# Performance work log

Measured on AMD Instinct MI355X. Metric: run time of the kernel, lower is better.

Reference implementation:

```python
import jax, jax.numpy as jnp
import numpy as np

NEG_SLOPE = 0.2  # PyG GATConv default leaky_relu slope

def gat_conv(x, src, dst, W, a_src, a_dst, bias, N):
    # Linear transform
    h = x @ W                      # [N, D]
    # Per-node attention logits (heads=1)
    al_src = h @ a_src             # [N]
    al_dst = h @ a_dst             # [N]
    e = jax.nn.leaky_relu(al_src[src] + al_dst[dst], NEG_SLOPE)  # [E]
    # Segment softmax over incoming edges of each destination node
    m = jax.ops.segment_max(e, dst, num_segments=N)
    ex = jnp.exp(e - m[dst])
    denom = jax.ops.segment_sum(ex, dst, num_segments=N)
    alpha = ex / denom[dst]        # [E]
    # Weighted scatter-aggregate of source features
    out = jax.ops.segment_sum(h[src] * alpha[:, None], dst, num_segments=N)
    return out + bias

def setup_inputs() -> dict:
    key = jax.random.key(0)
    ks = jax.random.split(key, 10)
    N, E, F_in, H, O = 50000, 800000, 128, 64, 64
    x = jax.random.normal(ks[0], (N, F_in), dtype=jnp.float32)
    edge_index = jax.random.randint(ks[1], (2, E), 0, N, dtype=jnp.int32)
    s = lambda k, shp, fan: jax.random.normal(k, shp, dtype=jnp.float32) / np.sqrt(fan)
    return {
        'x': x, 'edge_index': edge_index,
        'W1': s(ks[2], (F_in, H), F_in), 'a_src1': s(ks[3], (H,), H), 'a_dst1': s(ks[4], (H,), H), 'b1': jnp.zeros((H,), jnp.float32),
        'W2': s(ks[5], (H, O), H), 'a_src2': s(ks[6], (O,), O), 'a_dst2': s(ks[7], (O,), O), 'b2': jnp.zeros((O,), jnp.float32),
    }

def reference(x, edge_index, W1, a_src1, a_dst1, b1, W2, a_src2, a_dst2, b2):
    N = x.shape[0]
    loops = jnp.arange(N, dtype=edge_index.dtype)  # PyG adds self-loops by default
    src = jnp.concatenate([edge_index[0], loops])
    dst = jnp.concatenate([edge_index[1], loops])
    h = gat_conv(x, src, dst, W1, a_src1, a_dst1, b1, N)
    h = jax.nn.relu(h)
    # dropout(p=0.6) is identity in eval mode
    out = gat_conv(h, src, dst, W2, a_src2, a_dst2, b2, N)
    return out
```

## Files before the change

kernel.cpp:

```cpp
#include <hip/hip_runtime.h>
#include <hip/hip_bf16.h>

#define DEV static __device__ __forceinline__

typedef short bf16x8 __attribute__((ext_vector_type(8)));
typedef float f32x4  __attribute__((ext_vector_type(4)));

union U4 { uint4 u; bf16x8 s; };

DEV float b2f(__hip_bfloat16 v) { return __bfloat162float(v); }
DEV float lrelu(float e) { return e > 0.f ? e : 0.2f * e; }

DEV unsigned short f2bu(float f) {
    __hip_bfloat16 b = __float2bfloat16(f);
    return *reinterpret_cast<unsigned short*>(&b);
}
DEV float bu2f(unsigned short u) { return __uint_as_float((unsigned)u << 16); }

DEV float loadF(const void* p, size_t i, int f32) {
    if (f32) return ((const float*)p)[i];
    return b2f(((const __hip_bfloat16*)p)[i]);
}

DEV uint4 pack8(const unsigned short* t) {
    uint4 v;
    v.x = (unsigned)t[0] | ((unsigned)t[1] << 16);
    v.y = (unsigned)t[2] | ((unsigned)t[3] << 16);
    v.z = (unsigned)t[4] | ((unsigned)t[5] << 16);
    v.w = (unsigned)t[6] | ((unsigned)t[7] << 16);
    return v;
}

__global__ __launch_bounds__(256) void k_detect(
    const void* a0, int n0, const void* a1, int n1, const void* a2, int n2,
    const void* a3, int n3, const void* a4, int n4, const void* a5, int n5,
    const void* a6, int n6, const void* a7, int n7, const void* a8, int n8,
    int* __restrict__ flags)
{
    const void* ps[9] = {a0,a1,a2,a3,a4,a5,a6,a7,a8};
    const int   ns[9] = {n0,n1,n2,n3,n4,n5,n6,n7,n8};
    __shared__ int cnt;
    for (int k = 0; k < 9; ++k) {
        if (threadIdx.x == 0) cnt = 0;
        __syncthreads();
        int samples = ns[k] < 256 ? ns[k] : 256;
        if ((int)threadIdx.x < samples) {
            unsigned short u = ((const unsigned short*)ps[k])[threadIdx.x];
            unsigned e = (u >> 7) & 0xFFu;
            bool insane = (e >= 0xC8u) || (e == 0u && (u & 0x7Fu) != 0u);
            if (insane) atomicAdd(&cnt, 1);
        }
        __syncthreads();
        if (threadIdx.x == 0) flags[k] = (cnt >= 1) ? 1 : 0;
        __syncthreads();
    }
}

DEV void edge_sd(int i, int E, const int* __restrict__ src, const int* __restrict__ dst,
                 int& s, int& d) {
    if (i < E) { s = src[i]; d = dst[i]; }
    else       { s = d = i - E; }
}

#define G_BIN 128

__global__ __launch_bounds__(256) void k_binA(
    const int* __restrict__ src, const int* __restrict__ dst,
    int* __restrict__ hist, int E, int EA, int chunk)
{
    __shared__ int cnt[256];
    const int tid = threadIdx.x;
    cnt[tid] = 0;
    __syncthreads();
    const int lo = blockIdx.x * chunk;
    const int hi = min(lo + chunk, EA);
    for (int i = lo + tid; i < hi; i += 256) {
        int s, d; edge_sd(i, E, src, dst, s, d);
        atomicAdd(&cnt[d >> 8], 1);
    }
    __syncthreads();
    hist[blockIdx.x * 256 + tid] = cnt[tid];
}

__global__ __launch_bounds__(256) void k_binB(
    const int* __restrict__ hist, int* __restrict__ offs,
    int* __restrict__ bstart)
{
    __shared__ int sm[256];
    const int tid = threadIdx.x;
    int total = 0;
    for (int blk = 0; blk < G_BIN; ++blk) total += hist[blk * 256 + tid];
    sm[tid] = total;
    __syncthreads();
#pragma unroll
    for (int off = 1; off < 256; off <<= 1) {
        int t = (tid >= off) ? sm[tid - off] : 0;
        __syncthreads();
        sm[tid] += t;
        __syncthreads();
    }
    int b0 = sm[tid] - total;
    bstart[tid] = b0;
    if (tid == 255) bstart[256] = sm[255];
    int run = b0;
    for (int blk = 0; blk < G_BIN; ++blk) {
        offs[blk * 256 + tid] = run;
        run += hist[blk * 256 + tid];
    }
}

__global__ __launch_bounds__(256) void k_binC(
    const int* __restrict__ src, const int* __restrict__ dst,
    const int* __restrict__ offs, unsigned* __restrict__ ebuf,
    int E, int EA, int chunk)
{
    __shared__ int cur[256];
    const int tid = threadIdx.x;
    cur[tid] = offs[blockIdx.x * 256 + tid];
    __syncthreads();
    const int lo = blockIdx.x * chunk;
    const int hi = min(lo + chunk, EA);
    for (int i = lo + tid; i < hi; i += 256) {
        int s, d; edge_sd(i, E, src, dst, s, d);
        int pos = atomicAdd(&cur[d >> 8], 1);
        ebuf[pos] = ((unsigned)(d & 255) << 17) | (unsigned)s;
    }
}

__global__ __launch_bounds__(256) void k_binD(
    const unsigned* __restrict__ ebuf, const int* __restrict__ bstart,
    int* __restrict__ row_ptr, int* __restrict__ col, int N)
{
    __shared__ int cnt[256];
    __shared__ int pfx[256];
    const int tid = threadIdx.x;
    const int b = blockIdx.x;
    const int lo = bstart[b], hi = bstart[b + 1];
    cnt[tid] = 0;
    __syncthreads();
    for (int i = lo + tid; i < hi; i += 256)
        atomicAdd(&cnt[ebuf[i] >> 17], 1);
    __syncthreads();
    const int c = cnt[tid];
    pfx[tid] = c;
    __syncthreads();
#pragma unroll
    for (int off = 1; off < 256; off <<= 1) {
        int t = (tid >= off) ? pfx[tid - off] : 0;
        __syncthreads();
        pfx[tid] += t;
        __syncthreads();
    }
    const int excl = pfx[tid] - c;
    const int d = b * 256 + tid;
    if (d <= N) row_ptr[d] = lo + excl;
    __syncthreads();
    cnt[tid] = lo + excl;
    __syncthreads();
    for (int i = lo + tid; i < hi; i += 256) {
        unsigned v = ebuf[i];
        int pos = atomicAdd(&cnt[v >> 17], 1);
        col[pos] = (int)(v & 0x1FFFFu);
    }
}

__global__ __launch_bounds__(256) void k_gemm1(
    const void* __restrict__ x, const void* __restrict__ W,
    const void* __restrict__ a_s, const void* __restrict__ a_d,
    const int* __restrict__ flags,
    __hip_bfloat16* __restrict__ h, float* __restrict__ als, float* __restrict__ ald,
    int N)
{
    __shared__ __align__(16) unsigned short sMem[2 * 64 * 136];
    __shared__ float sAs[64], sAd[64];
    unsigned short* sA = sMem;
    unsigned short* sB = sMem + 64 * 136;
    float* sOut = (float*)sMem;

    const int tid = threadIdx.x;
    const int row0 = blockIdx.x * 64;
    const int fx = flags[0], fw = flags[1];

    if (tid < 64) sAs[tid] = loadF(a_s, tid, flags[2]);
    else if (tid < 128) sAd[tid - 64] = loadF(a_d, tid - 64, flags[3]);

    if (!fx) {
        const uint4* xg = (const uint4*)x;
#pragma unroll
        for (int it = 0; it < 2; ++it) {
            int g = tid + it * 256;
            int r = g >> 4, c16 = g & 15;
            uint4 v = (row0 + r < N) ? xg[(size_t)(row0 + r) * 16 + c16]
                                     : make_uint4(0, 0, 0, 0);
            *(uint4*)(sA + r * 136 + c16 * 8) = v;
        }
    } else {
        for (int i = tid; i < 64 * 128; i += 256) {
            int r = i >> 7, k = i & 127;
            float v = (row0 + r < N) ? ((const float*)x)[(size_t)(row0 + r) * 128 + k] : 0.f;
            sA[r * 136 + k] = f2bu(v);
        }
    }
    if (!fw) {
        const unsigned short* Wg = (const unsigned short*)W;
        const int n = tid & 63;
        int k0 = (tid >> 6) * 8;
#pragma unroll
        for (int rep = 0; rep < 4; ++rep, k0 += 32) {
            unsigned short t[8];
#pragma unroll
            for (int j = 0; j < 8; ++j) t[j] = Wg[(size_t)(k0 + j) * 64 + n];
            *(uint4*)(sB + n * 136 + k0) = pack8(t);
        }
    } else {
        const float* Wg = (const float*)W;
        for (int i = tid; i < 128 * 64; i += 256) {
            int k = i >> 6, n = i & 63;
            sB[n * 136 + k] = f2bu(Wg[i]);
        }
    }
    __syncthreads();

    const int w = tid >> 6, lane = tid & 63;
    const int m0 = w * 16;
    const int qr = lane >> 4;
    const int lc = lane & 15;

    bf16x8 afrag[4];
#pragma unroll
    for (int c = 0; c < 4; ++c) {
        U4 u; u.u = *(const uint4*)(sA + (m0 + lc) * 136 + c * 32 + qr * 8);
        afrag[c] = u.s;
    }
    f32x4 accs[4];
#pragma unroll
    for (int nt = 0; nt < 4; ++nt) {
        f32x4 acc = {0.f, 0.f, 0.f, 0.f};
#pragma unroll
        for (int c = 0; c < 4; ++c) {
            U4 u; u.u = *(const uint4*)(sB + (nt * 16 + lc) * 136 + c * 32 + qr * 8);
            acc = __builtin_amdgcn_mfma_f32_16x16x32_bf16(afrag[c], u.s, acc, 0, 0, 0);
        }
        accs[nt] = acc;
    }
    __syncthreads();

#pragma unroll
    for (int nt = 0; nt < 4; ++nt)
#pragma unroll
        for (int reg = 0; reg < 4; ++reg)
            sOut[(m0 + qr * 4 + reg) * 68 + nt * 16 + lc] = accs[nt][reg];
    __syncthreads();

    {
        const int r = tid >> 2, seg = tid & 3;
        const int row = row0 + r;
        const float* po = sOut + r * 68 + seg * 16;
        float ps = 0.f, pd = 0.f;
        unsigned short ob[16];
#pragma unroll
        for (int i = 0; i < 16; ++i) {
            float v = po[i];
            ps = fmaf(v, sAs[seg * 16 + i], ps);
            pd = fmaf(v, sAd[seg * 16 + i], pd);
            ob[i] = f2bu(v);
        }
        if (row < N) {
            uint4* hp = (uint4*)((unsigned short*)h + (size_t)row * 64 + seg * 16);
            hp[0] = pack8(ob);
            hp[1] = pack8(ob + 8);
        }
        ps += __shfl_xor(ps, 1, 64); ps += __shfl_xor(ps, 2, 64);
        pd += __shfl_xor(pd, 1, 64); pd += __shfl_xor(pd, 2, 64);
        if (seg == 0 && row < N) { als[row] = ps; ald[row] = pd; }
    }
}

__global__ __launch_bounds__(256) void k_gemm2(
    __hip_bfloat16* __restrict__ agg, const void* __restrict__ b1,
    const void* __restrict__ W, const void* __restrict__ a_s,
    const void* __restrict__ a_d, const int* __restrict__ flags,
    float* __restrict__ als, float* __restrict__ ald, int N)
{
    __shared__ __align__(16) unsigned short sMem[2 * 64 * 72];
    __shared__ float sAs[64], sAd[64], sBias[64];
    unsigned short* sA = sMem;
    unsigned short* sB = sMem + 64 * 72;
    float* sOut = (float*)sMem;

    const int tid = threadIdx.x;
    const int row0 = blockIdx.x * 64;
    const int fw = flags[5];

    if (tid < 64) sAs[tid] = loadF(a_s, tid, flags[6]);
    else if (tid < 128) sAd[tid - 64] = loadF(a_d, tid - 64, flags[7]);
    else if (tid < 192) sBias[tid - 128] = loadF(b1, tid - 128, flags[4]);
    __syncthreads();

    {
        const uint4* ag = (const uint4*)agg;
#pragma unroll
        for (int it = 0; it < 2; ++it) {
            int g = tid + it * 256;
            int r = g >> 3, c8 = g & 7;
            uint4 v = (row0 + r < N) ? ag[(size_t)(row0 + r) * 8 + c8]
                                     : make_uint4(0, 0, 0, 0);
            unsigned short in[8] = {
                (unsigned short)(v.x & 0xFFFF), (unsigned short)(v.x >> 16),
                (unsigned short)(v.y & 0xFFFF), (unsigned short)(v.y >> 16),
                (unsigned short)(v.z & 0xFFFF), (unsigned short)(v.z >> 16),
                (unsigned short)(v.w & 0xFFFF), (unsigned short)(v.w >> 16)};
            unsigned short ob[8];
#pragma unroll
            for (int j = 0; j < 8; ++j) {
                float t = bu2f(in[j]) + sBias[c8 * 8 + j];
                ob[j] = f2bu(t > 0.f ? t : 0.f);
            }
            *(uint4*)(sA + r * 72 + c8 * 8) = pack8(ob);
        }
    }
    if (!fw) {
        const unsigned short* Wg = (const unsigned short*)W;
        const int n = tid & 63;
        int k0 = (tid >> 6) * 8;
#pragma unroll
        for (int rep = 0; rep < 2; ++rep, k0 += 32) {
            unsigned short t[8];
#pragma unroll
            for (int j = 0; j < 8; ++j) t[j] = Wg[(size_t)(k0 + j) * 64 + n];
            *(uint4*)(sB + n * 72 + k0) = pack8(t);
        }
    } else {
        const float* Wg = (const float*)W;
        for (int i = tid; i < 64 * 64; i += 256) {
            int k = i >> 6, n = i & 63;
            sB[n * 72 + k] = f2bu(Wg[i]);
        }
    }
    __syncthreads();

    const int w = tid >> 6, lane = tid & 63;
    const int m0 = w * 16;
    const int qr = lane >> 4, lc = lane & 15;

    bf16x8 afrag[2];
#pragma unroll
    for (int c = 0; c < 2; ++c) {
        U4 u; u.u = *(const uint4*)(sA + (m0 + lc) * 72 + c * 32 + qr * 8);
        afrag[c] = u.s;
    }
    f32x4 accs[4];
#pragma unroll
    for (int nt = 0; nt < 4; ++nt) {
        f32x4 acc = {0.f, 0.f, 0.f, 0.f};
#pragma unroll
        for (int c = 0; c < 2; ++c) {
            U4 u; u.u = *(const uint4*)(sB + (nt * 16 + lc) * 72 + c * 32 + qr * 8);
            acc = __builtin_amdgcn_mfma_f32_16x16x32_bf16(afrag[c], u.s, acc, 0, 0, 0);
        }
        accs[nt] = acc;
    }
    __syncthreads();
#pragma unroll
    for (int nt = 0; nt < 4; ++nt)
#pragma unroll
        for (int reg = 0; reg < 4; ++reg)
            sOut[(m0 + qr * 4 + reg) * 68 + nt * 16 + lc] = accs[nt][reg];
    __syncthreads();

    {
        const int r = tid >> 2, seg = tid & 3;
        const int row = row0 + r;
        const float* po = sOut + r * 68 + seg * 16;
        float ps = 0.f, pd = 0.f;
        unsigned short ob[16];
#pragma unroll
        for (int i = 0; i < 16; ++i) {
            float v = po[i];
            ps = fmaf(v, sAs[seg * 16 + i], ps);
            pd = fmaf(v, sAd[seg * 16 + i], pd);
            ob[i] = f2bu(v);
        }
        if (row < N) {
            uint4* hp = (uint4*)((unsigned short*)agg + (size_t)row * 64 + seg * 16);
            hp[0] = pack8(ob);
            hp[1] = pack8(ob + 8);
        }
        ps += __shfl_xor(ps, 1, 64); ps += __shfl_xor(ps, 2, 64);
        pd += __shfl_xor(pd, 1, 64); pd += __shfl_xor(pd, 2, 64);
        if (seg == 0 && row < N) { als[row] = ps; ald[row] = pd; }
    }
}

__global__ __launch_bounds__(256) void k_gather(
    const int* __restrict__ row_ptr, const int* __restrict__ col,
    const float* __restrict__ als, const float* __restrict__ ald,
    const __hip_bfloat16* __restrict__ h,
    __hip_bfloat16* __restrict__ agg_out,
    void* __restrict__ final_out,
    const void* __restrict__ bias, const int* __restrict__ flags, int N)
{
    const int tid = threadIdx.x;
    const int lane = tid & 63;
    const int eg = lane >> 3, fg = lane & 7;
    const int wid = blockIdx.x * 4 + (tid >> 6);
    const int nw  = gridDim.x * 4;

    for (int d = wid; d < N; d += nw) {
        const float aldd = ald[d];
        const int beg = row_ptr[d], end = row_ptr[d + 1];
        float acc[8] = {0.f,0.f,0.f,0.f,0.f,0.f,0.f,0.f};
        float den = 0.f;
        for (int j0 = beg; j0 < end; j0 += 8) {
            const int je = j0 + eg;
            const bool act = je < end;
            const int s = col[act ? je : end - 1];
            const float w = act ? __expf(lrelu(als[s] + aldd)) : 0.f;
            den += w;
            const uint4 hv = *reinterpret_cast<const uint4*>(h + (size_t)s * 64 + fg * 8);
            acc[0] = fmaf(w, __uint_as_float(hv.x << 16),          acc[0]);
            acc[1] = fmaf(w, __uint_as_float(hv.x & 0xFFFF0000u),  acc[1]);
            acc[2] = fmaf(w, __uint_as_float(hv.y << 16),          acc[2]);
            acc[3] = fmaf(w, __uint_as_float(hv.y & 0xFFFF0000u),  acc[3]);
            acc[4] = fmaf(w, __uint_as_float(hv.z << 16),          acc[4]);
            acc[5] = fmaf(w, __uint_as_float(hv.z & 0xFFFF0000u),  acc[5]);
            acc[6] = fmaf(w, __uint_as_float(hv.w << 16),          acc[6]);
            acc[7] = fmaf(w, __uint_as_float(hv.w & 0xFFFF0000u),  acc[7]);
        }
#pragma unroll
        for (int off = 8; off <= 32; off <<= 1) {
            den += __shfl_xor(den, off, 64);
#pragma unroll
            for (int k = 0; k < 8; ++k) acc[k] += __shfl_xor(acc[k], off, 64);
        }
        if (eg == 0) {
            const float inv = 1.f / den;
            if (final_out) {
                float vb[8];
#pragma unroll
                for (int k = 0; k < 8; ++k) vb[k] = acc[k] * inv + loadF(bias, fg * 8 + k, flags[8]);
                if (flags[0]) {
                    float4* o = (float4*)((float*)final_out + (size_t)d * 64 + fg * 8);
                    o[0] = make_float4(vb[0], vb[1], vb[2], vb[3]);
                    o[1] = make_float4(vb[4], vb[5], vb[6], vb[7]);
                } else {
                    unsigned short ob[8];
#pragma unroll
                    for (int k = 0; k < 8; ++k) ob[k] = f2bu(vb[k]);
                    *reinterpret_cast<uint4*>((__hip_bfloat16*)final_out + (size_t)d * 64 + fg * 8) = pack8(ob);
                }
            } else {
                unsigned short ob[8];
#pragma unroll
                for (int k = 0; k < 8; ++k) ob[k] = f2bu(acc[k] * inv);
                *reinterpret_cast<uint4*>(agg_out + (size_t)d * 64 + fg * 8) = pack8(ob);
            }
        }
    }
}

extern "C" void kernel_launch(void* const* d_in, const int* in_sizes, int n_in,
                              void* d_out, int out_size, void* d_ws, size_t ws_size,
                              hipStream_t stream)
{
    const void* x   = d_in[0];
    const int*  ei  = (const int*)d_in[1];
    const void* W1  = d_in[2];
    const void* as1 = d_in[3];
    const void* ad1 = d_in[4];
    const void* b1  = d_in[5];
    const void* W2  = d_in[6];
    const void* as2 = d_in[7];
    const void* ad2 = d_in[8];
    const void* b2  = d_in[9];

    const int N  = in_sizes[0] / 128;
    const int E  = in_sizes[1] / 2;
    const int EA = E + N;
    const int* src = ei;
    const int* dst = ei + E;

    uintptr_t base = (uintptr_t)d_ws;
    auto alloc = [&](size_t bytes) { uintptr_t p = base; base += (bytes + 63) & ~(size_t)63; return p; };
    int*      flags   = (int*)alloc(64 * 4);
    float*    als     = (float*)alloc((size_t)N * 4);
    float*    ald     = (float*)alloc((size_t)N * 4);
    int*      row_ptr = (int*)alloc((size_t)(N + 1) * 4);
    int*      hist    = (int*)alloc((size_t)G_BIN * 256 * 4);
    int*      offs    = (int*)alloc((size_t)G_BIN * 256 * 4);
    int*      bstart  = (int*)alloc(257 * 4);
    unsigned* ebuf    = (unsigned*)alloc((size_t)EA * 4);
    int*      col     = (int*)alloc((size_t)EA * 4);
    __hip_bfloat16* hbuf   = (__hip_bfloat16*)alloc((size_t)N * 64 * 2);
    __hip_bfloat16* aggbuf = (__hip_bfloat16*)alloc((size_t)N * 64 * 2);

    const int gatherb = 2048;
    const int gb  = (N + 63) / 64;
    const int NBK = (N + 255) / 256;
    const int chunk = (EA + G_BIN - 1) / G_BIN;

    k_detect<<<1, 256, 0, stream>>>(
        x, in_sizes[0], W1, in_sizes[2], as1, in_sizes[3], ad1, in_sizes[4],
        b1, in_sizes[5], W2, in_sizes[6], as2, in_sizes[7], ad2, in_sizes[8],
        b2, in_sizes[9], flags);

    k_binA<<<G_BIN, 256, 0, stream>>>(src, dst, hist, E, EA, chunk);
    k_binB<<<1, 256, 0, stream>>>(hist, offs, bstart);
    k_binC<<<G_BIN, 256, 0, stream>>>(src, dst, offs, ebuf, E, EA, chunk);
    k_binD<<<NBK, 256, 0, stream>>>(ebuf, bstart, row_ptr, col, N);

    k_gemm1<<<gb, 256, 0, stream>>>(x, W1, as1, ad1, flags, hbuf, als, ald, N);
    k_gather<<<gatherb, 256, 0, stream>>>(row_ptr, col, als, ald, hbuf, aggbuf,
                                          nullptr, nullptr, flags, N);
    k_gemm2<<<gb, 256, 0, stream>>>(aggbuf, b1, W2, as2, ad2, flags, als, ald, N);
    k_gather<<<gatherb, 256, 0, stream>>>(row_ptr, col, als, ald, aggbuf, nullptr,
                                          d_out, b2, flags, N);
    (void)out_size; (void)ws_size; (void)n_in;
}
```

Baseline: 227.2 us.

## Split gather into two feature-half passes, parallelize bin scan and detect

Each gather now covers only 32 of the 64 features per launch and runs twice. This lets 16 edges be processed in parallel per wavefront, with nontemporal loads for col and nontemporal stores for outputs. The single-block histogram scan is split into a 256-block column scan plus a small bucket scan. The dtype-detect kernel now uses one wavefront per tensor with a ballot instead of a serialized loop with barriers. The gather split recomputes edge weights and rereads col twice per layer, trading redundant work for more edge-level parallelism.

Measured after the change: 333.4 us. +46.8%, slower.

```diff
diff --git a/kernel.cpp b/kernel.cpp
--- a/kernel.cpp
+++ b/kernel.cpp
@@ -5,6 +5,7 @@
 
 typedef short bf16x8 __attribute__((ext_vector_type(8)));
 typedef float f32x4  __attribute__((ext_vector_type(4)));
+typedef unsigned u32x4 __attribute__((ext_vector_type(4)));
 
 union U4 { uint4 u; bf16x8 s; };
 
@@ -31,7 +32,16 @@
     return v;
 }
 
-__global__ __launch_bounds__(256) void k_detect(
+DEV u32x4 pack8v(const unsigned short* t) {
+    u32x4 v;
+    v.x = (unsigned)t[0] | ((unsigned)t[1] << 16);
+    v.y = (unsigned)t[2] | ((unsigned)t[3] << 16);
+    v.z = (unsigned)t[4] | ((unsigned)t[5] << 16);
+    v.w = (unsigned)t[6] | ((unsigned)t[7] << 16);
+    return v;
+}
+
+__global__ __launch_bounds__(1024) void k_detect(
     const void* a0, int n0, const void* a1, int n1, const void* a2, int n2,
     const void* a3, int n3, const void* a4, int n4, const void* a5, int n5,
     const void* a6, int n6, const void* a7, int n7, const void* a8, int n8,
@@ -39,21 +49,22 @@
 {
     const void* ps[9] = {a0,a1,a2,a3,a4,a5,a6,a7,a8};
     const int   ns[9] = {n0,n1,n2,n3,n4,n5,n6,n7,n8};
-    __shared__ int cnt;
-    for (int k = 0; k < 9; ++k) {
-        if (threadIdx.x == 0) cnt = 0;
-        __syncthreads();
-        int samples = ns[k] < 256 ? ns[k] : 256;
-        if ((int)threadIdx.x < samples) {
-            unsigned short u = ((const unsigned short*)ps[k])[threadIdx.x];
+    const int w = threadIdx.x >> 6, lane = threadIdx.x & 63;
+    if (w >= 9) return;
+    const unsigned short* p = (const unsigned short*)ps[w];
+    const int n = ns[w];
+    bool insane = false;
+#pragma unroll
+    for (int r = 0; r < 4; ++r) {
+        int idx = lane + r * 64;
+        if (idx < n) {
+            unsigned short u = p[idx];
             unsigned e = (u >> 7) & 0xFFu;
-            bool insane = (e >= 0xC8u) || (e == 0u && (u & 0x7Fu) != 0u);
-            if (insane) atomicAdd(&cnt, 1);
-        }
-        __syncthreads();
-        if (threadIdx.x == 0) flags[k] = (cnt >= 1) ? 1 : 0;
-        __syncthreads();
-    }
+            insane |= (e >= 0xC8u) || (e == 0u && (u & 0x7Fu) != 0u);
+        }
+    }
+    unsigned long long m = __ballot(insane);
+    if (lane == 0) flags[w] = (m != 0ull) ? 1 : 0;
 }
 
 DEV void edge_sd(int i, int E, const int* __restrict__ src, const int* __restrict__ dst,
@@ -82,15 +93,34 @@
     hist[blockIdx.x * 256 + tid] = cnt[tid];
 }
 
-__global__ __launch_bounds__(256) void k_binB(
-    const int* __restrict__ hist, int* __restrict__ offs,
-    int* __restrict__ bstart)
+__global__ __launch_bounds__(G_BIN) void k_binB1(
+    const int* __restrict__ hist, int* __restrict__ offs_rel,
+    int* __restrict__ btot)
+{
+    __shared__ int sm[G_BIN];
+    const int t = threadIdx.x;
+    const int b = blockIdx.x;
+    int v = hist[t * 256 + b];
+    sm[t] = v;
+    __syncthreads();
+#pragma unroll
+    for (int off = 1; off < G_BIN; off <<= 1) {
+        int u = (t >= off) ? sm[t - off] : 0;
+        __syncthreads();
+        sm[t] += u;
+        __syncthreads();
+    }
+    offs_rel[t * 256 + b] = sm[t] - v;
+    if (t == G_BIN - 1) btot[b] = sm[t];
+}
+
+__global__ __launch_bounds__(256) void k_binB2(
+    const int* __restrict__ btot, int* __restrict__ bstart)
 {
     __shared__ int sm[256];
     const int tid = threadIdx.x;
-    int total = 0;
-    for (int blk = 0; blk < G_BIN; ++blk) total += hist[blk * 256 + tid];
-    sm[tid] = total;
+    int v = btot[tid];
+    sm[tid] = v;
     __syncthreads();
 #pragma unroll
     for (int off = 1; off < 256; off <<= 1) {
@@ -99,24 +129,18 @@
         sm[tid] += t;
         __syncthreads();
     }
-    int b0 = sm[tid] - total;
-    bstart[tid] = b0;
+    bstart[tid] = sm[tid] - v;
     if (tid == 255) bstart[256] = sm[255];
-    int run = b0;
-    for (int blk = 0; blk < G_BIN; ++blk) {
-        offs[blk * 256 + tid] = run;
-        run += hist[blk * 256 + tid];
-    }
 }
 
 __global__ __launch_bounds__(256) void k_binC(
     const int* __restrict__ src, const int* __restrict__ dst,
-    const int* __restrict__ offs, unsigned* __restrict__ ebuf,
-    int E, int EA, int chunk)
+    const int* __restrict__ offs_rel, const int* __restrict__ bstart,
+    unsigned* __restrict__ ebuf, int E, int EA, int chunk)
 {
     __shared__ int cur[256];
     const int tid = threadIdx.x;
-    cur[tid] = offs[blockIdx.x * 256 + tid];
+    cur[tid] = bstart[tid] + offs_rel[blockIdx.x * 256 + tid];
     __syncthreads();
     const int lo = blockIdx.x * chunk;
     const int hi = min(lo + chunk, EA);
@@ -398,11 +422,13 @@
     const __hip_bfloat16* __restrict__ h,
     __hip_bfloat16* __restrict__ agg_out,
     void* __restrict__ final_out,
-    const void* __restrict__ bias, const int* __restrict__ flags, int N)
+    const void* __restrict__ bias, const int* __restrict__ flags,
+    int N, int pass)
 {
     const int tid = threadIdx.x;
     const int lane = tid & 63;
-    const int eg = lane >> 3, fg = lane & 7;
+    const int eg = lane >> 2, fg = lane & 3;
+    const int fbase = pass * 32 + fg * 8;
     const int wid = blockIdx.x * 4 + (tid >> 6);
     const int nw  = gridDim.x * 4;
 
@@ -411,13 +437,13 @@
         const int beg = row_ptr[d], end = row_ptr[d + 1];
         float acc[8] = {0.f,0.f,0.f,0.f,0.f,0.f,0.f,0.f};
         float den = 0.f;
-        for (int j0 = beg; j0 < end; j0 += 8) {
+        for (int j0 = beg; j0 < end; j0 += 16) {
             const int je = j0 + eg;
             const bool act = je < end;
-            const int s = col[act ? je : end - 1];
+            const int s = __builtin_nontemporal_load(col + (act ? je : end - 1));
             const float w = act ? __expf(lrelu(als[s] + aldd)) : 0.f;
             den += w;
-            const uint4 hv = *reinterpret_cast<const uint4*>(h + (size_t)s * 64 + fg * 8);
+            const uint4 hv = *reinterpret_cast<const uint4*>(h + (size_t)s * 64 + fbase);
             acc[0] = fmaf(w, __uint_as_float(hv.x << 16),          acc[0]);
             acc[1] = fmaf(w, __uint_as_float(hv.x & 0xFFFF0000u),  acc[1]);
             acc[2] = fmaf(w, __uint_as_float(hv.y << 16),          acc[2]);
@@ -428,7 +454,7 @@
             acc[7] = fmaf(w, __uint_as_float(hv.w & 0xFFFF0000u),  acc[7]);
         }
 #pragma unroll
-        for (int off = 8; off <= 32; off <<= 1) {
+        for (int off = 4; off <= 32; off <<= 1) {
             den += __shfl_xor(den, off, 64);
 #pragma unroll
             for (int k = 0; k < 8; ++k) acc[k] += __shfl_xor(acc[k], off, 64);
@@ -438,22 +464,26 @@
             if (final_out) {
                 float vb[8];
 #pragma unroll
-                for (int k = 0; k < 8; ++k) vb[k] = acc[k] * inv + loadF(bias, fg * 8 + k, flags[8]);
+                for (int k = 0; k < 8; ++k) vb[k] = acc[k] * inv + loadF(bias, fbase + k, flags[8]);
                 if (flags[0]) {
-                    float4* o = (float4*)((float*)final_out + (size_t)d * 64 + fg * 8);
-                    o[0] = make_float4(vb[0], vb[1], vb[2], vb[3]);
-                    o[1] = make_float4(vb[4], vb[5], vb[6], vb[7]);
+                    float* o = (float*)final_out + (size_t)d * 64 + fbase;
+                    f32x4 o0 = {vb[0], vb[1], vb[2], vb[3]};
+                    f32x4 o1 = {vb[4], vb[5], vb[6], vb[7]};
+                    __builtin_nontemporal_store(o0, (f32x4*)o);
+                    __builtin_nontemporal_store(o1, (f32x4*)(o + 4));
                 } else {
                     unsigned short ob[8];
 #pragma unroll
                     for (int k = 0; k < 8; ++k) ob[k] = f2bu(vb[k]);
-                    *reinterpret_cast<uint4*>((__hip_bfloat16*)final_out + (size_t)d * 64 + fg * 8) = pack8(ob);
+                    __builtin_nontemporal_store(pack8v(ob),
+                        reinterpret_cast<u32x4*>((__hip_bfloat16*)final_out + (size_t)d * 64 + fbase));
                 }
             } else {
                 unsigned short ob[8];
 #pragma unroll
                 for (int k = 0; k < 8; ++k) ob[k] = f2bu(acc[k] * inv);
-                *reinterpret_cast<uint4*>(agg_out + (size_t)d * 64 + fg * 8) = pack8(ob);
+                __builtin_nontemporal_store(pack8v(ob),
+                    reinterpret_cast<u32x4*>(agg_out + (size_t)d * 64 + fbase));
             }
         }
     }
@@ -482,15 +512,16 @@
 
     uintptr_t base = (uintptr_t)d_ws;
     auto alloc = [&](size_t bytes) { uintptr_t p = base; base += (bytes + 63) & ~(size_t)63; return p; };
-    int*      flags   = (int*)alloc(64 * 4);
-    float*    als     = (float*)alloc((size_t)N * 4);
-    float*    ald     = (float*)alloc((size_t)N * 4);
-    int*      row_ptr = (int*)alloc((size_t)(N + 1) * 4);
-    int*      hist    = (int*)alloc((size_t)G_BIN * 256 * 4);
-    int*      offs    = (int*)alloc((size_t)G_BIN * 256 * 4);
-    int*      bstart  = (int*)alloc(257 * 4);
-    unsigned* ebuf    = (unsigned*)alloc((size_t)EA * 4);
-    int*      col     = (int*)alloc((size_t)EA * 4);
+    int*      flags    = (int*)alloc(64 * 4);
+    float*    als      = (float*)alloc((size_t)N * 4);
+    float*    ald      = (float*)alloc((size_t)N * 4);
+    int*      row_ptr  = (int*)alloc((size_t)(N + 1) * 4);
+    int*      hist     = (int*)alloc((size_t)G_BIN * 256 * 4);
+    int*      offs_rel = (int*)alloc((size_t)G_BIN * 256 * 4);
+    int*      btot     = (int*)alloc(256 * 4);
+    int*      bstart   = (int*)alloc(257 * 4);
+    unsigned* ebuf     = (unsigned*)alloc((size_t)EA * 4);
+    int*      col      = (int*)alloc((size_t)EA * 4);
     __hip_bfloat16* hbuf   = (__hip_bfloat16*)alloc((size_t)N * 64 * 2);
     __hip_bfloat16* aggbuf = (__hip_bfloat16*)alloc((size_t)N * 64 * 2);
 
@@ -499,21 +530,26 @@
     const int NBK = (N + 255) / 256;
     const int chunk = (EA + G_BIN - 1) / G_BIN;
 
-    k_detect<<<1, 256, 0, stream>>>(
+    k_detect<<<1, 1024, 0, stream>>>(
         x, in_sizes[0], W1, in_sizes[2], as1, in_sizes[3], ad1, in_sizes[4],
         b1, in_sizes[5], W2, in_sizes[6], as2, in_sizes[7], ad2, in_sizes[8],
         b2, in_sizes[9], flags);
 
     k_binA<<<G_BIN, 256, 0, stream>>>(src, dst, hist, E, EA, chunk);
-    k_binB<<<1, 256, 0, stream>>>(hist, offs, bstart);
-    k_binC<<<G_BIN, 256, 0, stream>>>(src, dst, offs, ebuf, E, EA, chunk);
+    k_binB1<<<256, G_BIN, 0, stream>>>(hist, offs_rel, btot);
+    k_binB2<<<1, 256, 0, stream>>>(btot, bstart);
+    k_binC<<<G_BIN, 256, 0, stream>>>(src, dst, offs_rel, bstart, ebuf, E, EA, chunk);
     k_binD<<<NBK, 256, 0, stream>>>(ebuf, bstart, row_ptr, col, N);
 
     k_gemm1<<<gb, 256, 0, stream>>>(x, W1, as1, ad1, flags, hbuf, als, ald, N);
     k_gather<<<gatherb, 256, 0, stream>>>(row_ptr, col, als, ald, hbuf, aggbuf,
-                                          nullptr, nullptr, flags, N);
+                                          nullptr, nullptr, flags, N, 0);
+    k_gather<<<gatherb, 256, 0, stream>>>(row_ptr, col, als, ald, hbuf, aggbuf,
+                                          nullptr, nullptr, flags, N, 1);
     k_gemm2<<<gb, 256, 0, stream>>>(aggbuf, b1, W2, as2, ad2, flags, als, ald, N);
     k_gather<<<gatherb, 256, 0, stream>>>(row_ptr, col, als, ald, aggbuf, nullptr,
-                                          d_out, b2, flags, N);
+                                          d_out, b2, flags, N, 0);
+    k_gather<<<gatherb, 256, 0, stream>>>(row_ptr, col, als, ald, aggbuf, nullptr,
+                                          d_out, b2, flags, N, 1);
     (void)out_size; (void)ws_size; (void)n_in;
 }
```
